# Optimization experiments

Measured on AMD Instinct MI355X. Metric: run time of the kernel, lower is better.

## Reference

```python
import jax, jax.numpy as jnp
import numpy as np

D, NH, L, P, FF = 256, 8, 3, 4, 1024
DH = D // NH
EPS = 1e-5

def _ln(x, g, b):
    m = jnp.mean(x, axis=-1, keepdims=True)
    v = jnp.mean((x - m) ** 2, axis=-1, keepdims=True)
    return (x - m) * jax.lax.rsqrt(v + EPS) * g + b

def _bilinear(value, loc, Hl, Wl):
    # value: [B,NH,Nl,DH]; loc (x,y) in [0,1]: [B,N,NH,P,2]; grid_sample align_corners=False, zero padding
    B, N = loc.shape[0], loc.shape[1]
    x = loc[..., 0] * Wl - 0.5
    y = loc[..., 1] * Hl - 0.5
    x0 = jnp.floor(x)
    y0 = jnp.floor(y)
    lx, ly = x - x0, y - y0
    x0 = x0.astype(jnp.int32)
    y0 = y0.astype(jnp.int32)

    def gather(xi, yi):
        valid = ((xi >= 0) & (xi < Wl) & (yi >= 0) & (yi < Hl)).astype(value.dtype)
        idx = jnp.clip(yi, 0, Hl - 1) * Wl + jnp.clip(xi, 0, Wl - 1)  # [B,N,NH,P]
        idx = idx.transpose(0, 2, 1, 3).reshape(B, NH, N * P, 1)
        v = jnp.take_along_axis(value, idx, axis=2)  # [B,NH,N*P,DH]
        v = v.reshape(B, NH, N, P, DH).transpose(0, 2, 1, 3, 4)  # [B,N,NH,P,DH]
        return v * valid[..., None]

    v00 = gather(x0, y0)
    v01 = gather(x0 + 1, y0)
    v10 = gather(x0, y0 + 1)
    v11 = gather(x0 + 1, y0 + 1)
    return (v00 * ((1 - lx) * (1 - ly))[..., None] + v01 * (lx * (1 - ly))[..., None]
            + v10 * ((1 - lx) * ly)[..., None] + v11 * (lx * ly)[..., None])

def _forward(query, p3, p4, p5, Wv, bv, Woff, boff, Wattn, battn, Wref, bref, Wo, bo,
             W1, b1, W2, b2, g1, be1, g2, be2, shapes):
    B, N, _ = query.shape
    off = (query @ Woff + boff).reshape(B, N, NH, L, P, 2)
    aw = jax.nn.softmax((query @ Wattn + battn).reshape(B, N, NH, L * P), axis=-1).reshape(B, N, NH, L, P)
    ref = jax.nn.sigmoid(query @ Wref + bref)[:, :, None, None, :]  # [B,N,1,1,2]
    out = jnp.zeros((B, N, NH, DH), query.dtype)
    for l, (feat, (Hl, Wl)) in enumerate(zip((p3, p4, p5), shapes)):
        val = (feat @ Wv + bv).reshape(B, Hl * Wl, NH, DH).transpose(0, 2, 1, 3)  # [B,NH,Nl,DH]
        loc = ref + off[:, :, :, l] / jnp.array([Wl, Hl], query.dtype)  # offsets normalized by (W,H)
        samp = _bilinear(val, loc, Hl, Wl)  # [B,N,NH,P,DH]
        out = out + jnp.einsum('bnhp,bnhpd->bnhd', aw[:, :, :, l], samp)
    attn_out = out.reshape(B, N, D) @ Wo + bo
    q = _ln(query + attn_out, g1, be1)  # residual + norm1 (dropout=eval identity)
    ffn = jax.nn.gelu(q @ W1 + b1, approximate=False) @ W2 + b2
    return _ln(q + ffn, g2, be2)

def setup_inputs():
    key = jax.random.key(0)
    ks = jax.random.split(key, 12)
    B = 4
    H3, W3, H4, W4, H5, W5 = 100, 100, 50, 50, 25, 25
    N = H3 * W3 + H4 * W4 + H5 * W5
    s = 0.02
    f32 = jnp.float32
    return dict(
        query=jax.random.normal(ks[0], (B, N, D), f32),
        p3=jax.random.normal(ks[1], (B, H3 * W3, D), f32),
        p4=jax.random.normal(ks[2], (B, H4 * W4, D), f32),
        p5=jax.random.normal(ks[3], (B, H5 * W5, D), f32),
        Wv=jax.random.normal(ks[4], (D, D), f32) * s, bv=jnp.zeros((D,), f32),
        Woff=jax.random.normal(ks[5], (D, NH * L * P * 2), f32) * s, boff=jnp.zeros((NH * L * P * 2,), f32),
        Wattn=jax.random.normal(ks[6], (D, NH * L * P), f32) * s, battn=jnp.zeros((NH * L * P,), f32),
        Wref=jax.random.normal(ks[7], (D, 2), f32) * s, bref=jnp.zeros((2,), f32),
        Wo=jax.random.normal(ks[8], (D, D), f32) * s, bo=jnp.zeros((D,), f32),
        W1=jax.random.normal(ks[9], (D, FF), f32) * s, b1=jnp.zeros((FF,), f32),
        W2=jax.random.normal(ks[10], (FF, D), f32) * s, b2=jnp.zeros((D,), f32),
        g1=jnp.ones((D,), f32), be1=jnp.zeros((D,), f32),
        g2=jnp.ones((D,), f32), be2=jnp.zeros((D,), f32),
        H3=H3, W3=W3, H4=H4, W4=W4, H5=H5, W5=W5,
    )

def reference(query, p3, p4, p5, Wv, bv, Woff, boff, Wattn, battn, Wref, bref, Wo, bo,
              W1, b1, W2, b2, g1, be1, g2, be2, H3, W3, H4, W4, H5, W5):
    return _forward(query, p3, p4, p5, Wv, bv, Woff, boff, Wattn, battn, Wref, bref, Wo, bo,
                    W1, b1, W2, b2, g1, be1, g2, be2, ((H3, W3), (H4, W4), (H5, W5)))
```

## Files before the change

### kernel.cpp

```cpp
#include <hip/hip_runtime.h>
#include <math.h>

#define BQ    4
#define NTOT  13125
#define DD    256
#define NHH   8
#define FFD   1024
#define EPSLN 1e-5f
#define MROWS (BQ * NTOT)
#define MPAD  52736

typedef __bf16 bf16_t;
typedef bf16_t bf16x8 __attribute__((ext_vector_type(8)));
typedef float floatx4 __attribute__((ext_vector_type(4)));

__device__ __forceinline__ unsigned short f2bf(float f) {
    unsigned u = __float_as_uint(f);
    return (unsigned short)((u + 0x7FFFu + ((u >> 16) & 1u)) >> 16);
}
__device__ __forceinline__ float bf2f(unsigned short h) {
    return __uint_as_float(((unsigned)h) << 16);
}

typedef const __attribute__((address_space(1))) unsigned int* gptr_t;
typedef __attribute__((address_space(3))) unsigned int* lptr_t;
__device__ __forceinline__ void gld16(const void* g, void* l) {
    __builtin_amdgcn_global_load_lds((gptr_t)g, (lptr_t)l, 16, 0, 0);
}

enum { EPI_F32 = 0, EPI_GELU = 2, EPI_VALSEG = 3 };

__device__ __forceinline__ int val_row(int gm) {
    if (gm < 40064) {
        if (gm >= 40000) return -1;
        int b = gm / 10000; int nl = gm - b * 10000;
        return b * NTOT + nl;
    } else if (gm < 50176) {
        int r = gm - 40064;
        if (r >= 10000) return -1;
        int b = r / 2500; int nl = r - b * 2500;
        return b * NTOT + 10000 + nl;
    } else {
        int r = gm - 50176;
        if (r >= 2500) return -1;
        int b = r / 625; int nl = r - b * 625;
        return b * NTOT + 12500 + nl;
    }
}

template <int EPI, typename OutT>
__launch_bounds__(256)
__global__ void mm_k(const unsigned short* __restrict__ A,
                     const unsigned short* __restrict__ Bt,
                     const float* __restrict__ bias, OutT* __restrict__ C,
                     int M, int K, int Nout, int ldc, int Mstore) {
    __shared__ __align__(16) unsigned short As[128 * 32];
    __shared__ __align__(16) unsigned short Bs[128 * 32];

    const int tid = threadIdx.x;
    const int m0 = blockIdx.x * 128;
    const int n0 = blockIdx.y * 128;
    const int w = tid >> 6, lane = tid & 63;
    const int q = lane >> 4, l15 = lane & 15;
    const int wm = (w & 1) * 64, wn = (w >> 1) * 64;

    const int sr = tid >> 2;
    const int sk = (tid & 3) * 8;

    const unsigned short* Ag = A + (size_t)(m0 + sr) * K + sk;
    const unsigned short* Bg = Bt + (size_t)(n0 + sr) * K + sk;
    char* AsB = (char*)As;
    char* BsB = (char*)Bs;

    floatx4 acc[4][4];
#pragma unroll
    for (int t = 0; t < 4; t++)
#pragma unroll
        for (int u = 0; u < 4; u++) {
            floatx4 z = {0.f, 0.f, 0.f, 0.f};
            acc[t][u] = z;
        }

    for (int k0 = 0; k0 < K; k0 += 32) {
        gld16(Ag + k0, AsB + tid * 16);
        gld16(Ag + (size_t)64 * K + k0, AsB + 4096 + tid * 16);
        gld16(Bg + k0, BsB + tid * 16);
        gld16(Bg + (size_t)64 * K + k0, BsB + 4096 + tid * 16);
        __syncthreads();

        bf16x8 af[4], bfr[4];
#pragma unroll
        for (int t = 0; t < 4; t++)
            af[t] = *reinterpret_cast<const bf16x8*>(&As[(wm + t * 16 + l15) * 32 + q * 8]);
#pragma unroll
        for (int u = 0; u < 4; u++)
            bfr[u] = *reinterpret_cast<const bf16x8*>(&Bs[(wn + u * 16 + l15) * 32 + q * 8]);
#pragma unroll
        for (int t = 0; t < 4; t++)
#pragma unroll
            for (int u = 0; u < 4; u++)
                acc[t][u] = __builtin_amdgcn_mfma_f32_16x16x32_bf16(af[t], bfr[u], acc[t][u], 0, 0, 0);
        __syncthreads();
    }

    float bias_v[4];
#pragma unroll
    for (int u = 0; u < 4; u++) {
        int gn = n0 + wn + u * 16 + l15;
        bias_v[u] = (gn < Nout) ? bias[gn] : 0.f;
    }

#pragma unroll
    for (int t = 0; t < 4; t++) {
#pragma unroll
        for (int r = 0; r < 4; r++) {
            int gm = m0 + wm + t * 16 + q * 4 + r;
            int orow = gm;
            if (EPI == EPI_VALSEG) orow = val_row(gm);
#pragma unroll
            for (int u = 0; u < 4; u++) {
                int gn = n0 + wn + u * 16 + l15;
                if (gn >= Nout) continue;
                float v = acc[t][u][r] + bias_v[u];
                if (EPI == EPI_GELU) {
                    v = 0.5f * v * (1.f + erff(v * 0.70710678118f));
                    if (gm < Mstore) {
                        float ov = (gm < M) ? v : 0.f;
                        ((unsigned short*)C)[(size_t)gm * ldc + gn] = f2bf(ov);
                    }
                } else if (EPI == EPI_VALSEG) {
                    if (orow >= 0)
                        ((unsigned short*)C)[(size_t)orow * ldc + gn] = f2bf(v);
                } else {
                    if (gm < M) ((float*)C)[(size_t)gm * ldc + gn] = v;
                }
            }
        }
    }
}

template <typename RT, typename OT>
__launch_bounds__(256)
__global__ void gemmln_k(const unsigned short* __restrict__ A,
                         const unsigned short* __restrict__ Bt,
                         const float* __restrict__ bias, const RT* __restrict__ res,
                         const float* __restrict__ g, const float* __restrict__ be,
                         OT* __restrict__ out, int M, int K) {
    __shared__ __align__(16) unsigned short As[64 * 32];
    __shared__ __align__(16) unsigned short Bs[256 * 32];

    const int tid = threadIdx.x;
    const int m0 = blockIdx.x * 64;
    const int w = tid >> 6, lane = tid & 63;
    const int q = lane >> 4, l15 = lane & 15;
    const int wn = w * 64;

    const int sr = tid >> 2;
    const int sk = (tid & 3) * 8;
    const unsigned short* Ag = A + (size_t)(m0 + sr) * K + sk;
    const unsigned short* Bg = Bt + (size_t)sr * K + sk;
    char* AsB = (char*)As;
    char* BsB = (char*)Bs;

    floatx4 acc[4][4];
#pragma unroll
    for (int t = 0; t < 4; t++)
#pragma unroll
        for (int u = 0; u < 4; u++) {
            floatx4 z = {0.f, 0.f, 0.f, 0.f};
            acc[t][u] = z;
        }

    for (int k0 = 0; k0 < K; k0 += 32) {
        gld16(Ag + k0, AsB + tid * 16);
#pragma unroll
        for (int j = 0; j < 4; j++)
            gld16(Bg + (size_t)j * 64 * K + k0, BsB + j * 4096 + tid * 16);
        __syncthreads();

        bf16x8 af[4], bfr[4];
#pragma unroll
        for (int t = 0; t < 4; t++)
            af[t] = *reinterpret_cast<const bf16x8*>(&As[(t * 16 + l15) * 32 + q * 8]);
#pragma unroll
        for (int u = 0; u < 4; u++)
            bfr[u] = *reinterpret_cast<const bf16x8*>(&Bs[(wn + u * 16 + l15) * 32 + q * 8]);
#pragma unroll
        for (int t = 0; t < 4; t++)
#pragma unroll
            for (int u = 0; u < 4; u++)
                acc[t][u] = __builtin_amdgcn_mfma_f32_16x16x32_bf16(af[t], bfr[u], acc[t][u], 0, 0, 0);
        __syncthreads();
    }

    float gg[4], bb[4], bias_v[4];
#pragma unroll
    for (int u = 0; u < 4; u++) {
        int gn = wn + u * 16 + l15;
        gg[u] = g[gn]; bb[u] = be[gn]; bias_v[u] = bias[gn];
    }

    float x[4][4][4];
    float ssum[4][4], ssq[4][4];
#pragma unroll
    for (int t = 0; t < 4; t++) {
#pragma unroll
        for (int r = 0; r < 4; r++) {
            int gm = m0 + t * 16 + q * 4 + r;
            bool valid = gm < M;
            float s = 0.f, sq = 0.f;
#pragma unroll
            for (int u = 0; u < 4; u++) {
                int gn = wn + u * 16 + l15;
                float rv = 0.f;
                if (valid) {
                    if (sizeof(RT) == 2)
                        rv = bf2f(((const unsigned short*)res)[(size_t)gm * DD + gn]);
                    else
                        rv = ((const float*)res)[(size_t)gm * DD + gn];
                }
                float xx = acc[t][u][r] + bias_v[u] + rv;
                x[t][r][u] = xx;
                s += xx; sq += xx * xx;
            }
            ssum[t][r] = s; ssq[t][r] = sq;
        }
    }
#pragma unroll
    for (int m = 1; m <= 8; m <<= 1) {
#pragma unroll
        for (int t = 0; t < 4; t++)
#pragma unroll
            for (int r = 0; r < 4; r++) {
                ssum[t][r] += __shfl_xor(ssum[t][r], m);
                ssq[t][r] += __shfl_xor(ssq[t][r], m);
            }
    }
    float* Ls = (float*)As;
    float* Lq = Ls + 256;
    if (l15 == 0) {
#pragma unroll
        for (int t = 0; t < 4; t++)
#pragma unroll
            for (int r = 0; r < 4; r++) {
                int lr = t * 16 + q * 4 + r;
                Ls[lr * 4 + w] = ssum[t][r];
                Lq[lr * 4 + w] = ssq[t][r];
            }
    }
    __syncthreads();

#pragma unroll
    for (int t = 0; t < 4; t++) {
#pragma unroll
        for (int r = 0; r < 4; r++) {
            int lr = t * 16 + q * 4 + r;
            int gm = m0 + lr;
            float tot = Ls[lr * 4 + 0] + Ls[lr * 4 + 1] + Ls[lr * 4 + 2] + Ls[lr * 4 + 3];
            float totq = Lq[lr * 4 + 0] + Lq[lr * 4 + 1] + Lq[lr * 4 + 2] + Lq[lr * 4 + 3];
            float mean = tot * (1.f / DD);
            float var = totq * (1.f / DD) - mean * mean;
            float rs = rsqrtf(var + EPSLN);
            if (gm < M) {
#pragma unroll
                for (int u = 0; u < 4; u++) {
                    int gn = wn + u * 16 + l15;
                    float o = (x[t][r][u] - mean) * rs * gg[u] + bb[u];
                    if (sizeof(OT) == 2)
                        ((unsigned short*)out)[(size_t)gm * DD + gn] = f2bf(o);
                    else
                        ((float*)out)[(size_t)gm * DD + gn] = o;
                }
            }
        }
    }
}

__launch_bounds__(512, 4)
__global__ void ffn_k(const unsigned short* __restrict__ A,
                      const unsigned short* __restrict__ Wt1,
                      const float* __restrict__ b1,
                      const unsigned short* __restrict__ Wt2,
                      const float* __restrict__ b2,
                      const float* __restrict__ g, const float* __restrict__ be,
                      float* __restrict__ out, int M) {
    __shared__ __align__(16) unsigned short qs[8 * 64 * 32];
    __shared__ __align__(16) unsigned short Hs[64 * 128];

    const int tid = threadIdx.x;
    const int m0 = blockIdx.x * 64;
    const int w = tid >> 6, lane = tid & 63;
    const int q = lane >> 4, l15 = lane & 15;

    {
        char* qsB = (char*)qs;
#pragma unroll
        for (int p = 0; p < 4; p++) {
            int idx = p * 8 + w;
            int kkb = idx >> 2;
            int row = (idx & 3) * 16 + (lane >> 2);
            int c = lane & 3;
            gld16(A + (size_t)(m0 + row) * 256 + kkb * 32 + c * 8,
                  qsB + idx * 1024 + lane * 16);
        }
    }

    floatx4 acc2[4][2];
#pragma unroll
    for (int t = 0; t < 4; t++)
#pragma unroll
        for (int u = 0; u < 2; u++) {
            floatx4 z = {0.f, 0.f, 0.f, 0.f};
            acc2[t][u] = z;
        }

    __syncthreads();

#pragma unroll 1
    for (int j = 0; j < 8; j++) {
        floatx4 acc1[4];
#pragma unroll
        for (int t = 0; t < 4; t++) {
            floatx4 z = {0.f, 0.f, 0.f, 0.f};
            acc1[t] = z;
        }
        const unsigned short* W1p = Wt1 + (size_t)(j * 128 + w * 16 + l15) * 256;
#pragma unroll
        for (int kk = 0; kk < 8; kk++) {
            bf16x8 af[4], bf1;
#pragma unroll
            for (int t = 0; t < 4; t++)
                af[t] = *reinterpret_cast<const bf16x8*>(&qs[kk * 2048 + (t * 16 + l15) * 32 + q * 8]);
            bf1 = *reinterpret_cast<const bf16x8*>(&W1p[kk * 32 + q * 8]);
#pragma unroll
            for (int t = 0; t < 4; t++)
                acc1[t] = __builtin_amdgcn_mfma_f32_16x16x32_bf16(af[t], bf1, acc1[t], 0, 0, 0);
        }
        __syncthreads();
        {
            int col = w * 16 + l15;
            float bv = b1[j * 128 + col];
#pragma unroll
            for (int t = 0; t < 4; t++)
#pragma unroll
                for (int r = 0; r < 4; r++) {
                    int row = t * 16 + q * 4 + r;
                    float v = acc1[t][r] + bv;
                    v = 0.5f * v * (1.f + erff(v * 0.70710678118f));
                    int bo = (row * 256 + col * 2) ^ ((row & 7) << 4);
                    *(unsigned short*)((char*)Hs + bo) = f2bf(v);
                }
        }
        __syncthreads();
        const unsigned short* W2p = Wt2 + (size_t)(w * 32) * 1024 + j * 128;
#pragma unroll
        for (int kk2 = 0; kk2 < 4; kk2++) {
            bf16x8 af2[4], bf2[2];
#pragma unroll
            for (int t = 0; t < 4; t++) {
                int row = t * 16 + l15;
                int bo = (row * 256 + (kk2 * 32 + q * 8) * 2) ^ ((row & 7) << 4);
                af2[t] = *reinterpret_cast<const bf16x8*>((const char*)Hs + bo);
            }
#pragma unroll
            for (int u = 0; u < 2; u++)
                bf2[u] = *reinterpret_cast<const bf16x8*>(&W2p[(size_t)(u * 16 + l15) * 1024 + kk2 * 32 + q * 8]);
#pragma unroll
            for (int t = 0; t < 4; t++)
#pragma unroll
                for (int u = 0; u < 2; u++)
                    acc2[t][u] = __builtin_amdgcn_mfma_f32_16x16x32_bf16(af2[t], bf2[u], acc2[t][u], 0, 0, 0);
        }
    }

    const int wn2 = w * 32;
    float gg[2], bb[2], bias_v[2];
#pragma unroll
    for (int u = 0; u < 2; u++) {
        int gn = wn2 + u * 16 + l15;
        gg[u] = g[gn]; bb[u] = be[gn]; bias_v[u] = b2[gn];
    }

    float x[4][4][2];
    float ssum[4][4], ssq[4][4];
#pragma unroll
    for (int t = 0; t < 4; t++) {
#pragma unroll
        for (int r = 0; r < 4; r++) {
            int row = t * 16 + q * 4 + r;
            float s = 0.f, sq = 0.f;
#pragma unroll
            for (int u = 0; u < 2; u++) {
                int gn = wn2 + u * 16 + l15;
                float rv = bf2f(qs[(gn >> 5) * 2048 + row * 32 + (gn & 31)]);
                float xx = acc2[t][u][r] + bias_v[u] + rv;
                x[t][r][u] = xx;
                s += xx; sq += xx * xx;
            }
            ssum[t][r] = s; ssq[t][r] = sq;
        }
    }
#pragma unroll
    for (int m = 1; m <= 8; m <<= 1) {
#pragma unroll
        for (int t = 0; t < 4; t++)
#pragma unroll
            for (int r = 0; r < 4; r++) {
                ssum[t][r] += __shfl_xor(ssum[t][r], m);
                ssq[t][r] += __shfl_xor(ssq[t][r], m);
            }
    }
    __syncthreads();
    float* Ls = (float*)qs;
    float* Lq = Ls + 512;
    if (l15 == 0) {
#pragma unroll
        for (int t = 0; t < 4; t++)
#pragma unroll
            for (int r = 0; r < 4; r++) {
                int lr = t * 16 + q * 4 + r;
                Ls[lr * 8 + w] = ssum[t][r];
                Lq[lr * 8 + w] = ssq[t][r];
            }
    }
    __syncthreads();

#pragma unroll
    for (int t = 0; t < 4; t++) {
#pragma unroll
        for (int r = 0; r < 4; r++) {
            int lr = t * 16 + q * 4 + r;
            int gm = m0 + lr;
            float tot = 0.f, totq = 0.f;
#pragma unroll
            for (int ww = 0; ww < 8; ww++) {
                tot += Ls[lr * 8 + ww];
                totq += Lq[lr * 8 + ww];
            }
            float mean = tot * (1.f / DD);
            float var = totq * (1.f / DD) - mean * mean;
            float rs = rsqrtf(var + EPSLN);
            if (gm < M) {
#pragma unroll
                for (int u = 0; u < 2; u++) {
                    int gn = wn2 + u * 16 + l15;
                    out[(size_t)gm * DD + gn] = (x[t][r][u] - mean) * rs * gg[u] + bb[u];
                }
            }
        }
    }
}

#define QELEMS   13500416
#define F3ELEMS  10256384
#define F4ELEMS   2588672
#define TOTELEMS 27000832

__launch_bounds__(256)
__global__ void cast_acts_k(const float* __restrict__ query, const float* __restrict__ p3,
                            const float* __restrict__ p4, const float* __restrict__ p5,
                            unsigned short* __restrict__ qbf, unsigned short* __restrict__ featsb) {
    int idx4 = (blockIdx.x * 256 + threadIdx.x) * 4;
    if (idx4 >= TOTELEMS) return;
    const float* src; unsigned short* dst; int local, real;
    if (idx4 < QELEMS) {
        src = query; dst = qbf; local = idx4; real = 13440000;
    } else {
        int j = idx4 - QELEMS;
        if (j < F3ELEMS)              { src = p3; dst = featsb;                    local = j;            real = 10240000; }
        else if (j < F3ELEMS + F4ELEMS){ src = p4; dst = featsb + F3ELEMS;         local = j - F3ELEMS;  real = 2560000; }
        else                          { src = p5; dst = featsb + F3ELEMS + F4ELEMS; local = j - F3ELEMS - F4ELEMS; real = 640000; }
    }
    float4 v = make_float4(0.f, 0.f, 0.f, 0.f);
    if (local < real) v = *(const float4*)&src[local];
    ushort4 o;
    o.x = f2bf(v.x); o.y = f2bf(v.y); o.z = f2bf(v.z); o.w = f2bf(v.w);
    *(ushort4*)&dst[local] = o;
}

#define WTQ_E   98304
#define WTV_E   (WTQ_E + 65536)
#define WTO_E   (WTV_E + 65536)
#define WT1_E   (WTO_E + 262144)
#define WT2_E   (WT1_E + 262144)
#define PREP_TOT (WT2_E + 384)

__launch_bounds__(256)
__global__ void prep_w_k(const float* __restrict__ Woff, const float* __restrict__ Wattn,
                         const float* __restrict__ Wref, const float* __restrict__ Wv,
                         const float* __restrict__ Wo, const float* __restrict__ W1,
                         const float* __restrict__ W2, const float* __restrict__ boff,
                         const float* __restrict__ battn, const float* __restrict__ bref,
                         unsigned short* __restrict__ warena, float* __restrict__ biasq) {
    int i = blockIdx.x * 256 + threadIdx.x;
    if (i >= PREP_TOT) return;
    if (i >= WT2_E) {
        int t = i - WT2_E;
        biasq[t] = (t < 192) ? boff[t] : (t < 288 ? battn[t - 192] : (t < 290 ? bref[t - 288] : 0.f));
        return;
    }
    float v;
    if (i < WTQ_E) {
        int n = i >> 8, k = i & 255;
        v = (n < 192) ? Woff[k * 192 + n]
          : (n < 288) ? Wattn[k * 96 + (n - 192)]
          : (n < 290) ? Wref[k * 2 + (n - 288)] : 0.f;
    } else if (i < WTV_E) {
        int j = i - WTQ_E; int n = j >> 8, k = j & 255;
        v = Wv[k * 256 + n];
    } else if (i < WTO_E) {
        int j = i - WTV_E; int n = j >> 8, k = j & 255;
        v = Wo[k * 256 + n];
    } else if (i < WT1_E) {
        int j = i - WTO_E; int n = j >> 8, k = j & 255;
        v = W1[k * 1024 + n];
    } else {
        int j = i - WT1_E; int n = j >> 10, k = j & 1023;
        v = W2[k * 256 + n];
    }
    warena[i] = f2bf(v);
}

__launch_bounds__(256)
__global__ void softmax12_k(const float* __restrict__ projb, unsigned short* __restrict__ aw) {
    int rh = blockIdx.x * 256 + threadIdx.x;
    if (rh >= MROWS * NHH) return;
    int bn = rh >> 3, h = rh & 7;
    const float* p = projb + (size_t)bn * 320 + 192 + h * 12;
    float v[12], mx = -1e30f;
#pragma unroll
    for (int i = 0; i < 12; i++) { v[i] = p[i]; mx = fmaxf(mx, v[i]); }
    float s = 0.f;
#pragma unroll
    for (int i = 0; i < 12; i++) { v[i] = expf(v[i] - mx); s += v[i]; }
    float inv = 1.f / s;
    unsigned short* o = aw + (size_t)rh * 12;
#pragma unroll
    for (int i = 0; i < 12; i++) o[i] = f2bf(v[i] * inv);
}

__launch_bounds__(128)
__global__ void sample_k(const unsigned short* __restrict__ val, const float* __restrict__ projb,
                         const unsigned short* __restrict__ aw,
                         unsigned short* __restrict__ out) {
    const int wv = threadIdx.x >> 6;
    const int lane = threadIdx.x & 63;
    const int bn = blockIdx.x * 2 + wv;
    const int b = bn / NTOT;
    __shared__ uint2 sc[2][96][4];

    const float* prow = projb + (size_t)bn * 320;
    float rx = 1.f / (1.f + expf(-prow[288]));
    float ry = 1.f / (1.f + expf(-prow[289]));
    for (int s0 = lane; s0 < 96; s0 += 64) {
        const int lp = s0 % 12;
        const int l = lp >> 2;
        int Hl, Wl, loff;
        if (l == 0)      { Hl = 100; Wl = 100; loff = 0; }
        else if (l == 1) { Hl = 50;  Wl = 50;  loff = 10000; }
        else             { Hl = 25;  Wl = 25;  loff = 12500; }
        float ox = prow[s0 * 2 + 0];
        float oy = prow[s0 * 2 + 1];
        float a  = bf2f(aw[(size_t)bn * 96 + s0]);
        float x = rx * (float)Wl + ox - 0.5f;
        float y = ry * (float)Hl + oy - 0.5f;
        x = fminf(fmaxf(x, -1e4f), 1e4f);
        y = fminf(fmaxf(y, -1e4f), 1e4f);
        float x0f = floorf(x), y0f = floorf(y);
        float lx = x - x0f, ly = y - y0f;
        int x0 = (int)x0f, y0 = (int)y0f;
#pragma unroll
        for (int c = 0; c < 4; c++) {
            int xi = x0 + (c & 1);
            int yi = y0 + (c >> 1);
            bool ok = (xi >= 0) && (xi < Wl) && (yi >= 0) && (yi < Hl);
            int xc = min(max(xi, 0), Wl - 1);
            int yc = min(max(yi, 0), Hl - 1);
            int idx = b * NTOT + loff + yc * Wl + xc;
            float wgt = ((c & 1) ? lx : 1.f - lx) * ((c >> 1) ? ly : 1.f - ly);
            sc[wv][s0][c] = make_uint2(__float_as_uint(ok ? a * wgt : 0.f), (unsigned)(idx * 512));
        }
    }
    __syncthreads();

    const int h = lane >> 3;
    const int dq = (lane & 7) * 4;
    const char* vb = (const char*)val + h * 64 + dq * 2;
    float a0 = 0.f, a1 = 0.f, a2 = 0.f, a3 = 0.f;
#pragma unroll
    for (int lp = 0; lp < 12; lp++) {
        int s = h * 12 + lp;
#pragma unroll
        for (int c = 0; c < 4; c++) {
            uint2 p = sc[wv][s][c];
            float wgt = __uint_as_float(p.x);
            uint2 u = *(const uint2*)(vb + p.y);
            a0 += wgt * __uint_as_float(u.x << 16);
            a1 += wgt * __uint_as_float(u.x & 0xFFFF0000u);
            a2 += wgt * __uint_as_float(u.y << 16);
            a3 += wgt * __uint_as_float(u.y & 0xFFFF0000u);
        }
    }
    uint2 ov;
    ov.x = (unsigned)f2bf(a0) | ((unsigned)f2bf(a1) << 16);
    ov.y = (unsigned)f2bf(a2) | ((unsigned)f2bf(a3) << 16);
    *(uint2*)(out + (size_t)bn * DD + h * 32 + dq) = ov;
}

extern "C" void kernel_launch(void* const* d_in, const int* in_sizes, int n_in,
                              void* d_out, int out_size, void* d_ws, size_t ws_size,
                              hipStream_t stream) {
    const float* query = (const float*)d_in[0];
    const float* p3    = (const float*)d_in[1];
    const float* p4    = (const float*)d_in[2];
    const float* p5    = (const float*)d_in[3];
    const float* Wv    = (const float*)d_in[4];
    const float* bv    = (const float*)d_in[5];
    const float* Woff  = (const float*)d_in[6];
    const float* boff  = (const float*)d_in[7];
    const float* Wattn = (const float*)d_in[8];
    const float* battn = (const float*)d_in[9];
    const float* Wref  = (const float*)d_in[10];
    const float* bref  = (const float*)d_in[11];
    const float* Wo    = (const float*)d_in[12];
    const float* bo    = (const float*)d_in[13];
    const float* W1    = (const float*)d_in[14];
    const float* b1    = (const float*)d_in[15];
    const float* W2    = (const float*)d_in[16];
    const float* b2    = (const float*)d_in[17];
    const float* g1    = (const float*)d_in[18];
    const float* be1   = (const float*)d_in[19];
    const float* g2    = (const float*)d_in[20];
    const float* be2   = (const float*)d_in[21];
    float* outp = (float*)d_out;

    char* wsb = (char*)d_ws;
    unsigned short* qbf    = (unsigned short*)(wsb + 0);
    float*          projb  = (float*)(wsb + 27000832);
    unsigned short* awb    = (unsigned short*)(wsb + 94502912);
    unsigned short* featsb = (unsigned short*)(wsb + 104582912);
    unsigned short* valb   = (unsigned short*)(wsb + 131583744);
    unsigned short* sampb  = (unsigned short*)(wsb + 158463744);
    unsigned short* warena = (unsigned short*)(wsb + 185399296);
    float*          biasq  = (float*)(wsb + 186906624);

    unsigned short* Wtq = warena;
    unsigned short* Wtv = warena + WTQ_E;
    unsigned short* Wto = warena + WTV_E;
    unsigned short* Wt1 = warena + WTO_E;
    unsigned short* Wt2 = warena + WT1_E;

    cast_acts_k<<<dim3(TOTELEMS / 4 / 256), 256, 0, stream>>>(query, p3, p4, p5, qbf, featsb);
    prep_w_k<<<dim3((PREP_TOT + 255) / 256), 256, 0, stream>>>(
        Woff, Wattn, Wref, Wv, Wo, W1, W2, boff, battn, bref, warena, biasq);
    mm_k<EPI_F32, float><<<dim3(MPAD / 128, 3), 256, 0, stream>>>(
        qbf, Wtq, biasq, projb, MROWS, 256, 290, 320, 0);
    softmax12_k<<<dim3((MROWS * NHH + 255) / 256), 256, 0, stream>>>(projb, awb);
    mm_k<EPI_VALSEG, unsigned short><<<dim3(MPAD / 128, 2), 256, 0, stream>>>(
        featsb, Wtv, bv, valb, 0, 256, 256, 256, 0);
    sample_k<<<dim3(MROWS / 2), 128, 0, stream>>>(valb, projb, awb, sampb);
    gemmln_k<float, unsigned short><<<dim3((MROWS + 63) / 64), 256, 0, stream>>>(
        sampb, Wto, bo, query, g1, be1, qbf, MROWS, 256);
    ffn_k<<<dim3((MROWS + 63) / 64), 512, 0, stream>>>(
        qbf, Wt1, b1, Wt2, b2, g2, be2, outp, MROWS);
}
```

Measured before the change: 553.0 us.

## Double-buffer FFN hidden tile and software-pipeline GEMM1 with GEMM2

Hidden-activation shared buffer is doubled so GEMM1 for chunk j can run interleaved with GEMM2 for chunk j-1, with GELU stores going to the alternate buffer. This reduces barriers per iteration from two to one and lets MFMA work from both GEMMs overlap LDS/global latency. It costs an extra 16KB of LDS per block, which may reduce occupancy under the 512-thread, 4-block launch bound, and raises register pressure.

New measurement: 560.2 us. Within noise of the previous version (+1.3%).

```diff
diff --git a/kernel.cpp b/kernel.cpp
--- a/kernel.cpp
+++ b/kernel.cpp
@@ -285,7 +285,7 @@
                       const float* __restrict__ g, const float* __restrict__ be,
                       float* __restrict__ out, int M) {
     __shared__ __align__(16) unsigned short qs[8 * 64 * 32];
-    __shared__ __align__(16) unsigned short Hs[64 * 128];
+    __shared__ __align__(16) unsigned short Hs[2][64 * 128];
 
     const int tid = threadIdx.x;
     const int m0 = blockIdx.x * 64;
@@ -314,15 +314,11 @@
             acc2[t][u] = z;
         }
 
-    __syncthreads();
-
-#pragma unroll 1
-    for (int j = 0; j < 8; j++) {
-        floatx4 acc1[4];
+    auto gemm1 = [&](int j, floatx4* a1) {
 #pragma unroll
         for (int t = 0; t < 4; t++) {
             floatx4 z = {0.f, 0.f, 0.f, 0.f};
-            acc1[t] = z;
+            a1[t] = z;
         }
         const unsigned short* W1p = Wt1 + (size_t)(j * 128 + w * 16 + l15) * 256;
 #pragma unroll
@@ -334,24 +330,28 @@
             bf1 = *reinterpret_cast<const bf16x8*>(&W1p[kk * 32 + q * 8]);
 #pragma unroll
             for (int t = 0; t < 4; t++)
-                acc1[t] = __builtin_amdgcn_mfma_f32_16x16x32_bf16(af[t], bf1, acc1[t], 0, 0, 0);
-        }
-        __syncthreads();
-        {
-            int col = w * 16 + l15;
-            float bv = b1[j * 128 + col];
-#pragma unroll
-            for (int t = 0; t < 4; t++)
-#pragma unroll
-                for (int r = 0; r < 4; r++) {
-                    int row = t * 16 + q * 4 + r;
-                    float v = acc1[t][r] + bv;
-                    v = 0.5f * v * (1.f + erff(v * 0.70710678118f));
-                    int bo = (row * 256 + col * 2) ^ ((row & 7) << 4);
-                    *(unsigned short*)((char*)Hs + bo) = f2bf(v);
-                }
-        }
-        __syncthreads();
+                a1[t] = __builtin_amdgcn_mfma_f32_16x16x32_bf16(af[t], bf1, a1[t], 0, 0, 0);
+        }
+    };
+
+    auto gelu_store = [&](int j, const floatx4* a1) {
+        char* Hp = (char*)Hs[j & 1];
+        int col = w * 16 + l15;
+        float bv = b1[j * 128 + col];
+#pragma unroll
+        for (int t = 0; t < 4; t++)
+#pragma unroll
+            for (int r = 0; r < 4; r++) {
+                int row = t * 16 + q * 4 + r;
+                float v = a1[t][r] + bv;
+                v = 0.5f * v * (1.f + erff(v * 0.70710678118f));
+                int bo = (row * 256 + col * 2) ^ ((row & 7) << 4);
+                *(unsigned short*)(Hp + bo) = f2bf(v);
+            }
+    };
+
+    auto gemm2 = [&](int j) {
+        const char* Hp = (const char*)Hs[j & 1];
         const unsigned short* W2p = Wt2 + (size_t)(w * 32) * 1024 + j * 128;
 #pragma unroll
         for (int kk2 = 0; kk2 < 4; kk2++) {
@@ -360,7 +360,7 @@
             for (int t = 0; t < 4; t++) {
                 int row = t * 16 + l15;
                 int bo = (row * 256 + (kk2 * 32 + q * 8) * 2) ^ ((row & 7) << 4);
-                af2[t] = *reinterpret_cast<const bf16x8*>((const char*)Hs + bo);
+                af2[t] = *reinterpret_cast<const bf16x8*>(Hp + bo);
             }
 #pragma unroll
             for (int u = 0; u < 2; u++)
@@ -371,7 +371,23 @@
                 for (int u = 0; u < 2; u++)
                     acc2[t][u] = __builtin_amdgcn_mfma_f32_16x16x32_bf16(af2[t], bf2[u], acc2[t][u], 0, 0, 0);
         }
-    }
+    };
+
+    __syncthreads();
+
+    floatx4 acc1[4];
+    gemm1(0, acc1);
+    gelu_store(0, acc1);
+    __syncthreads();
+
+#pragma unroll 1
+    for (int j = 1; j < 8; ++j) {
+        gemm1(j, acc1);
+        gemm2(j - 1);
+        gelu_store(j, acc1);
+        __syncthreads();
+    }
+    gemm2(7);
 
     const int wn2 = w * 32;
     float gg[2], bb[2], bias_v[2];
```

## Fuse output projection and first LayerNorm into FFN kernel

Applied to the files above, without the earlier changes.

The separate gemm+LayerNorm kernel for the attention output projection is removed, and that work now runs at the start of the FFN kernel. Each block loads its sampled rows into shared memory, multiplies them by Wo, adds the bias and the fp32 query residual, applies LayerNorm across the 8 waves, and writes the normalized bf16 rows back into the same shared buffer for the FFN. This drops one kernel launch and the global write and reread of the intermediate activation. In exchange the FFN kernel gains extra register pressure and barriers, and its Wo operands are read straight from global memory rather than staged through shared memory.

After: 596.2 us. +7.8%, slower.

```diff
diff --git a/kernel.cpp b/kernel.cpp
--- a/kernel.cpp
+++ b/kernel.cpp
@@ -139,158 +139,26 @@
     }
 }
 
-template <typename RT, typename OT>
-__launch_bounds__(256)
-__global__ void gemmln_k(const unsigned short* __restrict__ A,
-                         const unsigned short* __restrict__ Bt,
-                         const float* __restrict__ bias, const RT* __restrict__ res,
-                         const float* __restrict__ g, const float* __restrict__ be,
-                         OT* __restrict__ out, int M, int K) {
-    __shared__ __align__(16) unsigned short As[64 * 32];
-    __shared__ __align__(16) unsigned short Bs[256 * 32];
+__launch_bounds__(512, 4)
+__global__ void ffn_k(const unsigned short* __restrict__ S,
+                      const float* __restrict__ query,
+                      const unsigned short* __restrict__ Wto,
+                      const float* __restrict__ bo,
+                      const float* __restrict__ g1, const float* __restrict__ be1,
+                      const unsigned short* __restrict__ Wt1,
+                      const float* __restrict__ b1,
+                      const unsigned short* __restrict__ Wt2,
+                      const float* __restrict__ b2,
+                      const float* __restrict__ g2, const float* __restrict__ be2,
+                      float* __restrict__ out, int M) {
+    __shared__ __align__(16) unsigned short qs[8 * 64 * 32];
+    __shared__ __align__(16) unsigned short Hs[64 * 128];
 
     const int tid = threadIdx.x;
     const int m0 = blockIdx.x * 64;
     const int w = tid >> 6, lane = tid & 63;
     const int q = lane >> 4, l15 = lane & 15;
-    const int wn = w * 64;
-
-    const int sr = tid >> 2;
-    const int sk = (tid & 3) * 8;
-    const unsigned short* Ag = A + (size_t)(m0 + sr) * K + sk;
-    const unsigned short* Bg = Bt + (size_t)sr * K + sk;
-    char* AsB = (char*)As;
-    char* BsB = (char*)Bs;
-
-    floatx4 acc[4][4];
-#pragma unroll
-    for (int t = 0; t < 4; t++)
-#pragma unroll
-        for (int u = 0; u < 4; u++) {
-            floatx4 z = {0.f, 0.f, 0.f, 0.f};
-            acc[t][u] = z;
-        }
-
-    for (int k0 = 0; k0 < K; k0 += 32) {
-        gld16(Ag + k0, AsB + tid * 16);
-#pragma unroll
-        for (int j = 0; j < 4; j++)
-            gld16(Bg + (size_t)j * 64 * K + k0, BsB + j * 4096 + tid * 16);
-        __syncthreads();
-
-        bf16x8 af[4], bfr[4];
-#pragma unroll
-        for (int t = 0; t < 4; t++)
-            af[t] = *reinterpret_cast<const bf16x8*>(&As[(t * 16 + l15) * 32 + q * 8]);
-#pragma unroll
-        for (int u = 0; u < 4; u++)
-            bfr[u] = *reinterpret_cast<const bf16x8*>(&Bs[(wn + u * 16 + l15) * 32 + q * 8]);
-#pragma unroll
-        for (int t = 0; t < 4; t++)
-#pragma unroll
-            for (int u = 0; u < 4; u++)
-                acc[t][u] = __builtin_amdgcn_mfma_f32_16x16x32_bf16(af[t], bfr[u], acc[t][u], 0, 0, 0);
-        __syncthreads();
-    }
-
-    float gg[4], bb[4], bias_v[4];
-#pragma unroll
-    for (int u = 0; u < 4; u++) {
-        int gn = wn + u * 16 + l15;
-        gg[u] = g[gn]; bb[u] = be[gn]; bias_v[u] = bias[gn];
-    }
-
-    float x[4][4][4];
-    float ssum[4][4], ssq[4][4];
-#pragma unroll
-    for (int t = 0; t < 4; t++) {
-#pragma unroll
-        for (int r = 0; r < 4; r++) {
-            int gm = m0 + t * 16 + q * 4 + r;
-            bool valid = gm < M;
-            float s = 0.f, sq = 0.f;
-#pragma unroll
-            for (int u = 0; u < 4; u++) {
-                int gn = wn + u * 16 + l15;
-                float rv = 0.f;
-                if (valid) {
-                    if (sizeof(RT) == 2)
-                        rv = bf2f(((const unsigned short*)res)[(size_t)gm * DD + gn]);
-                    else
-                        rv = ((const float*)res)[(size_t)gm * DD + gn];
-                }
-                float xx = acc[t][u][r] + bias_v[u] + rv;
-                x[t][r][u] = xx;
-                s += xx; sq += xx * xx;
-            }
-            ssum[t][r] = s; ssq[t][r] = sq;
-        }
-    }
-#pragma unroll
-    for (int m = 1; m <= 8; m <<= 1) {
-#pragma unroll
-        for (int t = 0; t < 4; t++)
-#pragma unroll
-            for (int r = 0; r < 4; r++) {
-                ssum[t][r] += __shfl_xor(ssum[t][r], m);
-                ssq[t][r] += __shfl_xor(ssq[t][r], m);
-            }
-    }
-    float* Ls = (float*)As;
-    float* Lq = Ls + 256;
-    if (l15 == 0) {
-#pragma unroll
-        for (int t = 0; t < 4; t++)
-#pragma unroll
-            for (int r = 0; r < 4; r++) {
-                int lr = t * 16 + q * 4 + r;
-                Ls[lr * 4 + w] = ssum[t][r];
-                Lq[lr * 4 + w] = ssq[t][r];
-            }
-    }
-    __syncthreads();
-
-#pragma unroll
-    for (int t = 0; t < 4; t++) {
-#pragma unroll
-        for (int r = 0; r < 4; r++) {
-            int lr = t * 16 + q * 4 + r;
-            int gm = m0 + lr;
-            float tot = Ls[lr * 4 + 0] + Ls[lr * 4 + 1] + Ls[lr * 4 + 2] + Ls[lr * 4 + 3];
-            float totq = Lq[lr * 4 + 0] + Lq[lr * 4 + 1] + Lq[lr * 4 + 2] + Lq[lr * 4 + 3];
-            float mean = tot * (1.f / DD);
-            float var = totq * (1.f / DD) - mean * mean;
-            float rs = rsqrtf(var + EPSLN);
-            if (gm < M) {
-#pragma unroll
-                for (int u = 0; u < 4; u++) {
-                    int gn = wn + u * 16 + l15;
-                    float o = (x[t][r][u] - mean) * rs * gg[u] + bb[u];
-                    if (sizeof(OT) == 2)
-                        ((unsigned short*)out)[(size_t)gm * DD + gn] = f2bf(o);
-                    else
-                        ((float*)out)[(size_t)gm * DD + gn] = o;
-                }
-            }
-        }
-    }
-}
-
-__launch_bounds__(512, 4)
-__global__ void ffn_k(const unsigned short* __restrict__ A,
-                      const unsigned short* __restrict__ Wt1,
-                      const float* __restrict__ b1,
-                      const unsigned short* __restrict__ Wt2,
-                      const float* __restrict__ b2,
-                      const float* __restrict__ g, const float* __restrict__ be,
-                      float* __restrict__ out, int M) {
-    __shared__ __align__(16) unsigned short qs[8 * 64 * 32];
-    __shared__ __align__(16) unsigned short Hs[64 * 128];
-
-    const int tid = threadIdx.x;
-    const int m0 = blockIdx.x * 64;
-    const int w = tid >> 6, lane = tid & 63;
-    const int q = lane >> 4, l15 = lane & 15;
+    const int wn2 = w * 32;
 
     {
         char* qsB = (char*)qs;
@@ -300,10 +168,111 @@
             int kkb = idx >> 2;
             int row = (idx & 3) * 16 + (lane >> 2);
             int c = lane & 3;
-            gld16(A + (size_t)(m0 + row) * 256 + kkb * 32 + c * 8,
+            gld16(S + (size_t)(m0 + row) * 256 + kkb * 32 + c * 8,
                   qsB + idx * 1024 + lane * 16);
         }
     }
+    __syncthreads();
+
+    floatx4 acc0[4][2];
+#pragma unroll
+    for (int t = 0; t < 4; t++)
+#pragma unroll
+        for (int u = 0; u < 2; u++) {
+            floatx4 z = {0.f, 0.f, 0.f, 0.f};
+            acc0[t][u] = z;
+        }
+#pragma unroll
+    for (int kk = 0; kk < 8; kk++) {
+        bf16x8 af[4], bfo[2];
+#pragma unroll
+        for (int t = 0; t < 4; t++)
+            af[t] = *reinterpret_cast<const bf16x8*>(&qs[kk * 2048 + (t * 16 + l15) * 32 + q * 8]);
+#pragma unroll
+        for (int u = 0; u < 2; u++)
+            bfo[u] = *reinterpret_cast<const bf16x8*>(&Wto[(size_t)(wn2 + u * 16 + l15) * 256 + kk * 32 + q * 8]);
+#pragma unroll
+        for (int t = 0; t < 4; t++)
+#pragma unroll
+            for (int u = 0; u < 2; u++)
+                acc0[t][u] = __builtin_amdgcn_mfma_f32_16x16x32_bf16(af[t], bfo[u], acc0[t][u], 0, 0, 0);
+    }
+
+    float g1v[2], be1v[2], bov[2];
+#pragma unroll
+    for (int u = 0; u < 2; u++) {
+        int gn = wn2 + u * 16 + l15;
+        g1v[u] = g1[gn]; be1v[u] = be1[gn]; bov[u] = bo[gn];
+    }
+    float x0[4][4][2];
+    float ssum[4][4], ssq[4][4];
+#pragma unroll
+    for (int t = 0; t < 4; t++) {
+#pragma unroll
+        for (int r = 0; r < 4; r++) {
+            int row = t * 16 + q * 4 + r;
+            int gm = m0 + row;
+            bool valid = gm < M;
+            float s = 0.f, sq = 0.f;
+#pragma unroll
+            for (int u = 0; u < 2; u++) {
+                int gn = wn2 + u * 16 + l15;
+                float rv = valid ? query[(size_t)gm * DD + gn] : 0.f;
+                float xx = acc0[t][u][r] + bov[u] + rv;
+                x0[t][r][u] = xx;
+                s += xx; sq += xx * xx;
+            }
+            ssum[t][r] = s; ssq[t][r] = sq;
+        }
+    }
+#pragma unroll
+    for (int m = 1; m <= 8; m <<= 1) {
+#pragma unroll
+        for (int t = 0; t < 4; t++)
+#pragma unroll
+            for (int r = 0; r < 4; r++) {
+                ssum[t][r] += __shfl_xor(ssum[t][r], m);
+                ssq[t][r] += __shfl_xor(ssq[t][r], m);
+            }
+    }
+    __syncthreads();
+    {
+        float* Ls = (float*)Hs;
+        float* Lq = Ls + 512;
+        if (l15 == 0) {
+#pragma unroll
+            for (int t = 0; t < 4; t++)
+#pragma unroll
+                for (int r = 0; r < 4; r++) {
+                    int lr = t * 16 + q * 4 + r;
+                    Ls[lr * 8 + w] = ssum[t][r];
+                    Lq[lr * 8 + w] = ssq[t][r];
+                }
+        }
+        __syncthreads();
+#pragma unroll
+        for (int t = 0; t < 4; t++) {
+#pragma unroll
+            for (int r = 0; r < 4; r++) {
+                int lr = t * 16 + q * 4 + r;
+                float tot = 0.f, totq = 0.f;
+#pragma unroll
+                for (int ww = 0; ww < 8; ww++) {
+                    tot += Ls[lr * 8 + ww];
+                    totq += Lq[lr * 8 + ww];
+                }
+                float mean = tot * (1.f / DD);
+                float var = totq * (1.f / DD) - mean * mean;
+                float rs = rsqrtf(var + EPSLN);
+#pragma unroll
+                for (int u = 0; u < 2; u++) {
+                    float o = (x0[t][r][u] - mean) * rs * g1v[u] + be1v[u];
+                    qs[w * 2048 + lr * 32 + u * 16 + l15] = f2bf(o);
+                }
+            }
+        }
+    }
+    __syncthreads();
 
     floatx4 acc2[4][2];
 #pragma unroll
@@ -313,8 +282,6 @@
             floatx4 z = {0.f, 0.f, 0.f, 0.f};
             acc2[t][u] = z;
         }
-
-    __syncthreads();
 
 #pragma unroll 1
     for (int j = 0; j < 8; j++) {
@@ -347,20 +314,20 @@
                     int row = t * 16 + q * 4 + r;
                     float v = acc1[t][r] + bv;
                     v = 0.5f * v * (1.f + erff(v * 0.70710678118f));
-                    int bo = (row * 256 + col * 2) ^ ((row & 7) << 4);
-                    *(unsigned short*)((char*)Hs + bo) = f2bf(v);
+                    int bo2 = (row * 256 + col * 2) ^ ((row & 7) << 4);
+                    *(unsigned short*)((char*)Hs + bo2) = f2bf(v);
                 }
         }
         __syncthreads();
-        const unsigned short* W2p = Wt2 + (size_t)(w * 32) * 1024 + j * 128;
+        const unsigned short* W2p = Wt2 + (size_t)wn2 * 1024 + j * 128;
 #pragma unroll
         for (int kk2 = 0; kk2 < 4; kk2++) {
             bf16x8 af2[4], bf2[2];
 #pragma unroll
             for (int t = 0; t < 4; t++) {
                 int row = t * 16 + l15;
-                int bo = (row * 256 + (kk2 * 32 + q * 8) * 2) ^ ((row & 7) << 4);
-                af2[t] = *reinterpret_cast<const bf16x8*>((const char*)Hs + bo);
+                int bo2 = (row * 256 + (kk2 * 32 + q * 8) * 2) ^ ((row & 7) << 4);
+                af2[t] = *reinterpret_cast<const bf16x8*>((const char*)Hs + bo2);
             }
 #pragma unroll
             for (int u = 0; u < 2; u++)
@@ -373,16 +340,14 @@
         }
     }
 
-    const int wn2 = w * 32;
     float gg[2], bb[2], bias_v[2];
 #pragma unroll
     for (int u = 0; u < 2; u++) {
         int gn = wn2 + u * 16 + l15;
-        gg[u] = g[gn]; bb[u] = be[gn]; bias_v[u] = b2[gn];
+        gg[u] = g2[gn]; bb[u] = be2[gn]; bias_v[u] = b2[gn];
     }
 
     float x[4][4][2];
-    float ssum[4][4], ssq[4][4];
 #pragma unroll
     for (int t = 0; t < 4; t++) {
 #pragma unroll
@@ -659,8 +624,6 @@
     mm_k<EPI_VALSEG, unsigned short><<<dim3(MPAD / 128, 2), 256, 0, stream>>>(
         featsb, Wtv, bv, valb, 0, 256, 256, 256, 0);
     sample_k<<<dim3(MROWS / 2), 128, 0, stream>>>(valb, projb, awb, sampb);
-    gemmln_k<float, unsigned short><<<dim3((MROWS + 63) / 64), 256, 0, stream>>>(
-        sampb, Wto, bo, query, g1, be1, qbf, MROWS, 256);
     ffn_k<<<dim3((MROWS + 63) / 64), 512, 0, stream>>>(
-        qbf, Wt1, b1, Wt2, b2, g2, be2, outp, MROWS);
-}
+        sampb, query, Wto, bo, g1, be1, Wt1, b1, Wt2, b2, g2, be2, outp, MROWS);
+}
```
